# Kernel tuning notes

Measured on AMD Instinct MI355X. Metric: run time of the kernel, lower is better.

The kernel has to match this reference:

```python
import jax, jax.numpy as jnp
import numpy as np

N = 16384
D = 512
VOCAB = 100000
EMB_SCALE = 0.05  # keep dot products ~O(1) so exp() is stable, like trained embeddings


def setup_inputs() -> dict:
    key = jax.random.key(0)
    k1, k2, k3, k4 = jax.random.split(key, 4)
    input_emb = jax.random.normal(k1, (N, D), dtype=jnp.float32) * EMB_SCALE
    target_emb = jax.random.normal(k2, (N, D), dtype=jnp.float32) * EMB_SCALE
    target_ids = jax.random.randint(k3, (N,), 0, VOCAB, dtype=jnp.int64) if jax.config.jax_enable_x64 else jax.random.randint(k3, (N,), 0, VOCAB, dtype=jnp.int32)
    # sampling probabilities in (eps, ~0.5) so 1 - q stays well away from 0
    q_probas = jax.random.uniform(k4, (N,), dtype=jnp.float32, minval=1e-4, maxval=0.5)
    # first half positives, second half negatives (static pattern, matches boolean-mask semantics)
    mask = jnp.arange(N) < (N // 2)
    return {"input_emb": input_emb, "target_emb": target_emb, "target_ids": target_ids,
            "q_probas": q_probas, "mask": mask}


def reference(input_emb, target_emb, target_ids, q_probas, mask):
    # mask is a constant selection pattern -> resolve to static index lists (jit-friendly shapes)
    mask_np = np.asarray(mask)
    pos_idx = np.nonzero(mask_np)[0]
    neg_idx = np.nonzero(~mask_np)[0]

    pos_emb = input_emb[pos_idx]                      # [P, D]
    pos_tgt = target_emb[pos_idx]                     # [P, D]
    neg_tgt = target_emb[neg_idx]                     # [Q, D]

    pos_sim = jnp.einsum('pd,pd->p', pos_emb, pos_tgt)          # [P]
    neg_sim = jnp.einsum('pd,qd->pq', pos_emb, neg_tgt)         # [P, Q]

    # accidental-hit mask: 1 where negative id differs from the positive's true id
    miss = (target_ids[pos_idx][:, None] != target_ids[neg_idx]).astype(jnp.float32)  # [P, Q]
    n_miss = jnp.sum(miss, axis=1, keepdims=True)                # [P, 1]

    # logQ correction: subtract log(n_miss * q_neg / (1 - q_pos))
    log_q = jnp.log(n_miss * q_probas[neg_idx][None, :] / (1.0 - q_probas[pos_idx][:, None]))
    neg_exp = jnp.exp(neg_sim - log_q)                           # [P, Q]
    neg_exp_sum = jnp.einsum('pq,pq->p', miss, neg_exp)          # [P]

    pos_exp = jnp.exp(pos_sim)
    batch_loss = jnp.mean(-pos_sim + jnp.log(pos_exp + neg_exp_sum))
    return batch_loss
```

## Files before the change

kernel.cpp:

```cpp
#include <hip/hip_runtime.h>
#include <hip/hip_bf16.h>

#define NPOS 8192
#define NNEG 8192
#define DIM  512
#define VOCAB 100000

#define FP8_SCALE 64.0f
#define ACC_DESCALE (1.0f / 4096.0f)

typedef float f32x4 __attribute__((ext_vector_type(4)));
typedef long  lng2  __attribute__((ext_vector_type(2)));

__device__ __forceinline__ void async_load16(const void* g, void* l) {
    __builtin_amdgcn_global_load_lds(
        (const __attribute__((address_space(1))) void*)g,
        (__attribute__((address_space(3))) void*)l, 16, 0, 0);
}

__global__ void zero_kernel(int* __restrict__ hist, float* __restrict__ S) {
    const int t = blockIdx.x * 256 + threadIdx.x;
    if (t < VOCAB) hist[t] = 0;
    if (t < NPOS)  S[t] = 0.0f;
}

__global__ void prep_kernel(const float* __restrict__ input_emb,
                            const float* __restrict__ target_emb,
                            const int* __restrict__ ids,
                            const float* __restrict__ q_probas,
                            unsigned char* __restrict__ A8,
                            unsigned char* __restrict__ B8,
                            float* __restrict__ w, float* __restrict__ pos_sim,
                            int* __restrict__ hist) {
    const int r    = (blockIdx.x * blockDim.x + threadIdx.x) >> 6;
    const int lane = threadIdx.x & 63;

    const float4* ain = (const float4*)(input_emb  + (size_t)r * DIM);
    const float4* tin = (const float4*)(target_emb + (size_t)r * DIM);
    const float4* bin = (const float4*)(target_emb + (size_t)(NPOS + r) * DIM);

    float4 a0 = ain[lane * 2], a1 = ain[lane * 2 + 1];
    float4 t0 = tin[lane * 2], t1 = tin[lane * 2 + 1];
    float4 b0 = bin[lane * 2], b1 = bin[lane * 2 + 1];

    int alo = __builtin_amdgcn_cvt_pk_fp8_f32(a0.x * FP8_SCALE, a0.y * FP8_SCALE, 0, false);
    alo     = __builtin_amdgcn_cvt_pk_fp8_f32(a0.z * FP8_SCALE, a0.w * FP8_SCALE, alo, true);
    int ahi = __builtin_amdgcn_cvt_pk_fp8_f32(a1.x * FP8_SCALE, a1.y * FP8_SCALE, 0, false);
    ahi     = __builtin_amdgcn_cvt_pk_fp8_f32(a1.z * FP8_SCALE, a1.w * FP8_SCALE, ahi, true);
    int blo = __builtin_amdgcn_cvt_pk_fp8_f32(b0.x * FP8_SCALE, b0.y * FP8_SCALE, 0, false);
    blo     = __builtin_amdgcn_cvt_pk_fp8_f32(b0.z * FP8_SCALE, b0.w * FP8_SCALE, blo, true);
    int bhi = __builtin_amdgcn_cvt_pk_fp8_f32(b1.x * FP8_SCALE, b1.y * FP8_SCALE, 0, false);
    bhi     = __builtin_amdgcn_cvt_pk_fp8_f32(b1.z * FP8_SCALE, b1.w * FP8_SCALE, bhi, true);

    const int s = lane & 7, wnd = lane >> 3;
    const int phys = wnd * 64 + (s & 3) * 16 + (s >> 2) * 8;
    *(int2*)(A8 + (size_t)r * DIM + phys) = make_int2(alo, ahi);
    *(int2*)(B8 + (size_t)r * DIM + phys) = make_int2(blo, bhi);

    float sum = a0.x * t0.x + a0.y * t0.y + a0.z * t0.z + a0.w * t0.w
              + a1.x * t1.x + a1.y * t1.y + a1.z * t1.z + a1.w * t1.w;
    #pragma unroll
    for (int m = 32; m >= 1; m >>= 1) sum += __shfl_xor(sum, m);

    if (lane == 0) {
        pos_sim[r] = sum;
        w[r] = 1.0f / q_probas[NPOS + r];
        atomicAdd(&hist[ids[NPOS + r]], 1);
    }
}

__global__ __launch_bounds__(256) void gemm_kernel(
        const unsigned char* __restrict__ A8, const unsigned char* __restrict__ B8,
        const int* __restrict__ ids, const float* __restrict__ w,
        float* __restrict__ S) {
    __shared__ __align__(16) unsigned char Atile[128 * 64];
    __shared__ __align__(16) unsigned char Btile[128 * 64];

    const int tid  = threadIdx.x;
    const int lane = tid & 63;
    const int wv   = tid >> 6;
    const int wave_m = (wv & 1) * 64;
    const int wave_n = (wv >> 1) * 64;
    const int quad = lane >> 4;
    const int r16  = lane & 15;
    const int bm = blockIdx.x, bn = blockIdx.y;

    f32x4 acc[4][4] = {};

    const int srow_in = lane >> 2;
    const int sslot   = lane & 3;
    const size_t a_base = (size_t)(bm * 128) * DIM;
    const size_t b_base = (size_t)(bn * 128) * DIM;

    for (int k0 = 0; k0 < DIM; k0 += 64) {
        if (k0) __syncthreads();
        #pragma unroll
        for (int cc = 0; cc < 2; ++cc) {
            const int chunk = wv * 2 + cc;
            const int row = chunk * 16 + srow_in;
            const int g = sslot ^ (row & 3);
            async_load16(A8 + a_base + (size_t)row * DIM + k0 + g * 16,
                         Atile + chunk * 1024);
            async_load16(B8 + b_base + (size_t)row * DIM + k0 + g * 16,
                         Btile + chunk * 1024);
        }
        __syncthreads();

        lng2 af[4], bg[4];
        #pragma unroll
        for (int i = 0; i < 4; ++i) {
            const int arow = wave_m + i * 16 + r16;
            const int slot = quad ^ (r16 & 3);
            af[i] = *(const lng2*)(Atile + arow * 64 + slot * 16);
            const int brow = wave_n + i * 16 + r16;
            bg[i] = *(const lng2*)(Btile + brow * 64 + slot * 16);
        }
        #pragma unroll
        for (int i = 0; i < 4; ++i)
            #pragma unroll
            for (int j = 0; j < 4; ++j)
                acc[i][j] = __builtin_amdgcn_mfma_f32_16x16x32_fp8_fp8(af[i].x, bg[j].x, acc[i][j], 0, 0, 0);
        #pragma unroll
        for (int i = 0; i < 4; ++i)
            #pragma unroll
            for (int j = 0; j < 4; ++j)
                acc[i][j] = __builtin_amdgcn_mfma_f32_16x16x32_fp8_fp8(af[i].y, bg[j].y, acc[i][j], 0, 0, 0);
    }

    int idq[4]; float wq[4];
    #pragma unroll
    for (int j = 0; j < 4; ++j) {
        const int q = bn * 128 + wave_n + j * 16 + r16;
        idq[j] = ids[NPOS + q];
        wq[j]  = w[q];
    }
    #pragma unroll
    for (int i = 0; i < 4; ++i) {
        const int p0 = bm * 128 + wave_m + i * 16 + quad * 4;
        #pragma unroll
        for (int rr = 0; rr < 4; ++rr) {
            const int p = p0 + rr;
            const int idp = ids[p];
            float partial = 0.f;
            #pragma unroll
            for (int j = 0; j < 4; ++j) {
                const float e = __expf(acc[i][j][rr] * ACC_DESCALE) * wq[j];
                partial += (idp != idq[j]) ? e : 0.f;
            }
            partial += __shfl_xor(partial, 1);
            partial += __shfl_xor(partial, 2);
            partial += __shfl_xor(partial, 4);
            partial += __shfl_xor(partial, 8);
            if (r16 == 0) atomicAdd(&S[p], partial);
        }
    }
}

__global__ void final_kernel(const float* __restrict__ pos_sim,
                             const float* __restrict__ S,
                             const int* __restrict__ hist,
                             const int* __restrict__ ids,
                             const float* __restrict__ q_probas,
                             float* __restrict__ out) {
    __shared__ float red[256];
    float local = 0.f;
    for (int p = threadIdx.x; p < NPOS; p += 256) {
        const float ps  = pos_sim[p];
        const float n_miss = (float)(NNEG - hist[ids[p]]);
        const float nes = S[p] * (1.0f - q_probas[p]) / n_miss;
        local += -ps + logf(expf(ps) + nes);
    }
    red[threadIdx.x] = local;
    __syncthreads();
    #pragma unroll
    for (int s = 128; s > 0; s >>= 1) {
        if (threadIdx.x < s) red[threadIdx.x] += red[threadIdx.x + s];
        __syncthreads();
    }
    if (threadIdx.x == 0) out[0] = red[0] / (float)NPOS;
}

extern "C" void kernel_launch(void* const* d_in, const int* in_sizes, int n_in,
                              void* d_out, int out_size, void* d_ws, size_t ws_size,
                              hipStream_t stream) {
    const float* input_emb  = (const float*)d_in[0];
    const float* target_emb = (const float*)d_in[1];
    const int*   target_ids = (const int*)d_in[2];
    const float* q_probas   = (const float*)d_in[3];

    char* ws = (char*)d_ws;
    unsigned char* A8 = (unsigned char*)ws;
    unsigned char* B8 = (unsigned char*)(ws + (size_t)NPOS * DIM);
    float*  S       = (float*)(ws + (size_t)NPOS * DIM * 2);
    float*  w       = S + NPOS;
    float*  pos_sim = w + NPOS;
    int*    hist    = (int*)(pos_sim + NPOS);

    zero_kernel<<<(VOCAB + 255) / 256, 256, 0, stream>>>(hist, S);
    prep_kernel<<<2048, 256, 0, stream>>>(input_emb, target_emb, target_ids,
                                          q_probas, A8, B8, w, pos_sim, hist);
    gemm_kernel<<<dim3(64, 64), 256, 0, stream>>>(A8, B8, target_ids, w, S);
    final_kernel<<<1, 256, 0, stream>>>(pos_sim, S, hist, target_ids, q_probas, (float*)d_out);
}
```

Before: 210.9 us.

## Switch GEMM to MI355 scaled 16x16x128 FP8 MFMA with 128-wide K tiles

New measurement: 301.8 us. 1.43x slower.

```diff
diff --git a/kernel.cpp b/kernel.cpp
--- a/kernel.cpp
+++ b/kernel.cpp
@@ -8,9 +8,11 @@
 
 #define FP8_SCALE 64.0f
 #define ACC_DESCALE (1.0f / 4096.0f)
+#define SCALE_ONE 0x7F7F7F7F
 
 typedef float f32x4 __attribute__((ext_vector_type(4)));
-typedef long  lng2  __attribute__((ext_vector_type(2)));
+typedef int   i32x4 __attribute__((ext_vector_type(4)));
+typedef int   i32x8 __attribute__((ext_vector_type(8)));
 
 __device__ __forceinline__ void async_load16(const void* g, void* l) {
     __builtin_amdgcn_global_load_lds(
@@ -52,10 +54,8 @@
     int bhi = __builtin_amdgcn_cvt_pk_fp8_f32(b1.x * FP8_SCALE, b1.y * FP8_SCALE, 0, false);
     bhi     = __builtin_amdgcn_cvt_pk_fp8_f32(b1.z * FP8_SCALE, b1.w * FP8_SCALE, bhi, true);
 
-    const int s = lane & 7, wnd = lane >> 3;
-    const int phys = wnd * 64 + (s & 3) * 16 + (s >> 2) * 8;
-    *(int2*)(A8 + (size_t)r * DIM + phys) = make_int2(alo, ahi);
-    *(int2*)(B8 + (size_t)r * DIM + phys) = make_int2(blo, bhi);
+    *(int2*)(A8 + (size_t)r * DIM + lane * 8) = make_int2(alo, ahi);
+    *(int2*)(B8 + (size_t)r * DIM + lane * 8) = make_int2(blo, bhi);
 
     float sum = a0.x * t0.x + a0.y * t0.y + a0.z * t0.z + a0.w * t0.w
               + a1.x * t1.x + a1.y * t1.y + a1.z * t1.z + a1.w * t1.w;
@@ -73,8 +73,8 @@
         const unsigned char* __restrict__ A8, const unsigned char* __restrict__ B8,
         const int* __restrict__ ids, const float* __restrict__ w,
         float* __restrict__ S) {
-    __shared__ __align__(16) unsigned char Atile[128 * 64];
-    __shared__ __align__(16) unsigned char Btile[128 * 64];
+    __shared__ __align__(16) unsigned char Atile[128 * 128];
+    __shared__ __align__(16) unsigned char Btile[128 * 128];
 
     const int tid  = threadIdx.x;
     const int lane = tid & 63;
@@ -87,44 +87,45 @@
 
     f32x4 acc[4][4] = {};
 
-    const int srow_in = lane >> 2;
-    const int sslot   = lane & 3;
+    const int srow_in = lane >> 3;
+    const int sslot   = lane & 7;
     const size_t a_base = (size_t)(bm * 128) * DIM;
     const size_t b_base = (size_t)(bn * 128) * DIM;
 
-    for (int k0 = 0; k0 < DIM; k0 += 64) {
+    for (int k0 = 0; k0 < DIM; k0 += 128) {
         if (k0) __syncthreads();
         #pragma unroll
-        for (int cc = 0; cc < 2; ++cc) {
-            const int chunk = wv * 2 + cc;
-            const int row = chunk * 16 + srow_in;
-            const int g = sslot ^ (row & 3);
-            async_load16(A8 + a_base + (size_t)row * DIM + k0 + g * 16,
-                         Atile + chunk * 1024);
-            async_load16(B8 + b_base + (size_t)row * DIM + k0 + g * 16,
-                         Btile + chunk * 1024);
+        for (int cc = 0; cc < 4; ++cc) {
+            const int rblk = wv * 4 + cc;
+            const int row = rblk * 8 + srow_in;
+            const int c = sslot ^ (row & 7);
+            async_load16(A8 + a_base + (size_t)row * DIM + k0 + c * 16,
+                         Atile + rblk * 1024);
+            async_load16(B8 + b_base + (size_t)row * DIM + k0 + c * 16,
+                         Btile + rblk * 1024);
         }
         __syncthreads();
 
-        lng2 af[4], bg[4];
+        const int sr = r16 & 7;
+        const int slo = (2 * quad) ^ sr, shi = (2 * quad + 1) ^ sr;
+        i32x8 af[4], bg[4];
         #pragma unroll
         for (int i = 0; i < 4; ++i) {
-            const int arow = wave_m + i * 16 + r16;
-            const int slot = quad ^ (r16 & 3);
-            af[i] = *(const lng2*)(Atile + arow * 64 + slot * 16);
-            const int brow = wave_n + i * 16 + r16;
-            bg[i] = *(const lng2*)(Btile + brow * 64 + slot * 16);
+            const unsigned char* ab = Atile + (wave_m + i * 16 + r16) * 128;
+            i32x4 lo = *(const i32x4*)(ab + slo * 16);
+            i32x4 hi = *(const i32x4*)(ab + shi * 16);
+            af[i] = __builtin_shufflevector(lo, hi, 0, 1, 2, 3, 4, 5, 6, 7);
+            const unsigned char* bb = Btile + (wave_n + i * 16 + r16) * 128;
+            lo = *(const i32x4*)(bb + slo * 16);
+            hi = *(const i32x4*)(bb + shi * 16);
+            bg[i] = __builtin_shufflevector(lo, hi, 0, 1, 2, 3, 4, 5, 6, 7);
         }
         #pragma unroll
         for (int i = 0; i < 4; ++i)
             #pragma unroll
             for (int j = 0; j < 4; ++j)
-                acc[i][j] = __builtin_amdgcn_mfma_f32_16x16x32_fp8_fp8(af[i].x, bg[j].x, acc[i][j], 0, 0, 0);
-        #pragma unroll
-        for (int i = 0; i < 4; ++i)
-            #pragma unroll
-            for (int j = 0; j < 4; ++j)
-                acc[i][j] = __builtin_amdgcn_mfma_f32_16x16x32_fp8_fp8(af[i].y, bg[j].y, acc[i][j], 0, 0, 0);
+                acc[i][j] = __builtin_amdgcn_mfma_scale_f32_16x16x128_f8f6f4(
+                    af[i], bg[j], acc[i][j], 0, 0, 0, SCALE_ONE, 0, SCALE_ONE);
     }
 
     int idq[4]; float wq[4];
```
